# Kernel tuning notes

Measured on AMD Instinct MI355X. Metric: run time of the kernel, lower is better.

## Reference

```python
import jax, jax.numpy as jnp
import numpy as np

N_DRUG = 572
D = 512
K = 64          # neighbor_sample_size
T = 30000       # tail entities
R = 200         # relations
MAX_DEG = 32    # padded invariant_adj neighbor count
EPS = 1e-5


def setup_inputs() -> dict:
    key = jax.random.key(0)
    ks = jax.random.split(key, 10)
    return {
        "drug_embed_W": jax.random.normal(ks[0], (N_DRUG, D), jnp.float32),
        "rela_embed_W": jax.random.normal(ks[1], (R, D), jnp.float32),
        "ent_embed_W": jax.random.normal(ks[2], (T, D), jnp.float32),
        "Wa": jax.random.normal(ks[3], (D, D), jnp.float32) / np.float32(np.sqrt(D)),
        "lin_W": jax.random.normal(ks[4], (2 * D, D), jnp.float32) / np.float32(np.sqrt(2 * D)),
        "lin_b": jnp.zeros((D,), jnp.float32),
        "gamma": jnp.ones((D,), jnp.float32),
        "beta": jnp.zeros((D,), jnp.float32),
        "drug_name": jnp.arange(N_DRUG, dtype=jnp.int64 if jax.config.jax_enable_x64 else jnp.int32),
        "adj_tail": jax.random.randint(ks[5], (N_DRUG, K), 0, T),
        "adj_relation": jax.random.randint(ks[6], (N_DRUG, K), 0, R),
        "nbr_idx": jax.random.randint(ks[7], (N_DRUG, MAX_DEG), 0, N_DRUG),
        "nbr_deg": jax.random.randint(ks[8], (N_DRUG,), 0, MAX_DEG),
        "epoch": 2,
    }


def _forward(drug_embed_W, rela_embed_W, ent_embed_W, Wa, lin_W, lin_b, gamma, beta,
             drug_name, adj_tail, adj_relation, nbr_idx, nbr_deg, epoch):
    drug_e = drug_embed_W[drug_name]          # [N, D]
    rela = rela_embed_W[adj_relation]         # [N, K, D]
    ent = ent_embed_W[adj_tail]               # [N, K, D]

    # relation-aware attention over sampled neighbors (AttentionLayer)
    q = drug_e @ Wa                           # [N, D]
    scores = jnp.einsum('nd,nkd->nk', q, rela) * (1.0 / np.float32(np.sqrt(D)))
    attn = jax.nn.softmax(scores, axis=1)     # [N, K]
    agg = jnp.einsum('nk,nkd->nd', attn, ent) # [N, D]

    # Linear1: Linear(2D->D) + ReLU + BatchNorm1d (training-mode batch stats)
    h = jnp.concatenate([agg, drug_e], axis=1) @ lin_W + lin_b
    h = jax.nn.relu(h)
    mean = jnp.mean(h, axis=0)
    var = jnp.var(h, axis=0)                  # biased, as torch BN normalization
    drug_f = (h - mean) * jax.lax.rsqrt(var + EPS) * gamma + beta

    if epoch > 1:
        # sequential per-node neighbor-mean smoothing (in-place semantics)
        mask = (jnp.arange(MAX_DEG)[None, :] < nbr_deg[:, None])  # [N, MAX_DEG]

        def step(f, i):
            pos = nbr_idx[i]
            m = mask[i][:, None].astype(f.dtype)
            s = jnp.sum(f[pos] * m, axis=0)
            deg = nbr_deg[i]
            avg = s / jnp.maximum(deg, 1).astype(f.dtype)
            new = jnp.where(deg > 0, (avg + f[i]) * 0.5, f[i])
            return f.at[i].set(new), None

        drug_f, _ = jax.lax.scan(step, drug_f, jnp.arange(N_DRUG))
    return drug_f


def reference(drug_embed_W, rela_embed_W, ent_embed_W, Wa, lin_W, lin_b, gamma, beta,
              drug_name, adj_tail, adj_relation, nbr_idx, nbr_deg, epoch):
    return _forward(drug_embed_W, rela_embed_W, ent_embed_W, Wa, lin_W, lin_b, gamma, beta,
                    drug_name, adj_tail, adj_relation, nbr_idx, nbr_deg, epoch)
```

## Files before the change

### kernel.cpp

```cpp
#include <hip/hip_runtime.h>

#define N_DRUG 572
#define DIM 512
#define MAXDEG 32
#define FSB 12

__global__ __launch_bounds__(256) void prep_kernel(
    const float* __restrict__ Wa, const float* __restrict__ relaW,
    const float* __restrict__ linW, const int* __restrict__ nbr_idx,
    const int* __restrict__ nbr_deg, float* __restrict__ linP,
    float* __restrict__ relaP, int* __restrict__ sched_g)
{
    const int b = blockIdx.x;
    const int t = threadIdx.x;
    if (b < 512) {
        const int g = b * 256 + t;
        const int c = g & 511, k4 = g >> 9;
        const float4 v = make_float4(linW[(size_t)(k4 * 4 + 0) * 512 + c],
                                     linW[(size_t)(k4 * 4 + 1) * 512 + c],
                                     linW[(size_t)(k4 * 4 + 2) * 512 + c],
                                     linW[(size_t)(k4 * 4 + 3) * 512 + c]);
        *(float4*)&linP[((size_t)(c >> 6) * 256 + k4) * 256 + (c & 63) * 4] = v;
        return;
    }
    if (b == 928) {
        __shared__ int mxs2[N_DRUG];
        for (int i = t; i < N_DRUG; i += 256) {
            const int d = nbr_deg[i];
            const int4* np = (const int4*)&nbr_idx[i * MAXDEG];
            int mx = -1;
            #pragma unroll
            for (int u = 0; u < 8; ++u) {
                const int4 qq = np[u];
                const int bb = u * 4;
                mx = max(mx, (bb + 0 < d && qq.x < i) ? qq.x : -1);
                mx = max(mx, (bb + 1 < d && qq.y < i) ? qq.y : -1);
                mx = max(mx, (bb + 2 < d && qq.z < i) ? qq.z : -1);
                mx = max(mx, (bb + 3 < d && qq.w < i) ? qq.w : -1);
            }
            mxs2[i] = mx;
        }
        __syncthreads();
        if (t < 64) {
            int gs = 0, nr = 0;
            if (t == 0) sched_g[0] = 0;
            while (gs < N_DRUG) {
                const int jj = gs + 1 + t;
                const bool flag = (t >= 15) || (jj >= N_DRUG) ||
                                  (mxs2[min(jj, N_DRUG - 1)] >= gs);
                const int ge = gs + 1 + (int)__builtin_ctzll(__ballot(flag) & 0xFFFFULL);
                ++nr;
                if (t == 0) sched_g[nr] = ge;
                gs = ge;
            }
            if (t == 0) {
                sched_g[nr + 1] = N_DRUG;
                sched_g[nr + 2] = N_DRUG;
                sched_g[nr + 3] = N_DRUG;
            }
        }
        return;
    }
    const int bb = b - 512;
    const int rb = bb >> 5, kb = bb & 31;
    const int wv = t >> 6, l = t & 63;
    const int r0 = rb * 16 + wv * 4;
    const int k0 = kb * 16;

    float a[4][8];
    #pragma unroll
    for (int rr = 0; rr < 4; ++rr) {
        const float4* ap = (const float4*)(relaW + (size_t)min(r0 + rr, 199) * 512 + l * 8);
        const float4 x = ap[0], y = ap[1];
        a[rr][0] = x.x; a[rr][1] = x.y; a[rr][2] = x.z; a[rr][3] = x.w;
        a[rr][4] = y.x; a[rr][5] = y.y; a[rr][6] = y.z; a[rr][7] = y.w;
    }
    float acc[64];
    #pragma unroll
    for (int i = 0; i < 64; ++i) acc[i] = 0.f;
    #pragma unroll
    for (int kk = 0; kk < 16; ++kk) {
        const float4* bp = (const float4*)(Wa + (size_t)(k0 + kk) * 512 + l * 8);
        const float4 x = bp[0], y = bp[1];
        const float bv[8] = {x.x, x.y, x.z, x.w, y.x, y.y, y.z, y.w};
        #pragma unroll
        for (int rr = 0; rr < 4; ++rr) {
            float s = acc[rr * 16 + kk];
            #pragma unroll
            for (int j = 0; j < 8; ++j) s = fmaf(a[rr][j], bv[j], s);
            acc[rr * 16 + kk] = s;
        }
    }
    #pragma unroll
    for (int off = 1; off <= 32; off <<= 1) {
        #pragma unroll
        for (int i = 0; i < 64; ++i) acc[i] += __shfl_xor(acc[i], off, 64);
    }
    float outv = acc[0];
    #pragma unroll
    for (int i = 1; i < 64; ++i) outv = (l == i) ? acc[i] : outv;
    const int rr = l >> 4, kk = l & 15;
    if (r0 + rr < 200) relaP[(size_t)(r0 + rr) * 512 + k0 + kk] = outv;
}

__global__ __launch_bounds__(256) void attn_kernel(
    const float* __restrict__ drugW, const float* __restrict__ relaP,
    const float* __restrict__ entW, const int* __restrict__ dn,
    const int* __restrict__ adj_tail, const int* __restrict__ adj_rel,
    float* __restrict__ cat)
{
    __shared__ float at[64];
    __shared__ int tails[64];
    __shared__ int rels[64];
    const int d = blockIdx.x;
    const int t = threadIdx.x;
    const int w = t >> 6, lane = t & 63;

    if (t < 64) {
        tails[t] = adj_tail[d * 64 + t];
        rels[t]  = adj_rel[d * 64 + t];
    }
    const int rd = dn[d];
    float qv[8];
    {
        const float4* qp = (const float4*)(drugW + (size_t)rd * 512 + lane * 8);
        const float4 x = qp[0], y = qp[1];
        qv[0] = x.x; qv[1] = x.y; qv[2] = x.z; qv[3] = x.w;
        qv[4] = y.x; qv[5] = y.y; qv[6] = y.z; qv[7] = y.w;
    }
    __syncthreads();

    #pragma unroll 4
    for (int kk = 0; kk < 16; ++kk) {
        const int k = w * 16 + kk;
        const float4* p = (const float4*)(relaP + (size_t)rels[k] * 512 + lane * 8);
        const float4 x = p[0], y = p[1];
        float s = 0.f;
        s = fmaf(qv[0], x.x, s); s = fmaf(qv[1], x.y, s);
        s = fmaf(qv[2], x.z, s); s = fmaf(qv[3], x.w, s);
        s = fmaf(qv[4], y.x, s); s = fmaf(qv[5], y.y, s);
        s = fmaf(qv[6], y.z, s); s = fmaf(qv[7], y.w, s);
        #pragma unroll
        for (int off = 32; off >= 1; off >>= 1) s += __shfl_xor(s, off, 64);
        if (lane == 0) at[k] = s * 0.0441941738241592f;
    }
    __syncthreads();

    if (w == 0) {
        const float s = at[lane];
        float m = s;
        #pragma unroll
        for (int off = 32; off >= 1; off >>= 1) m = fmaxf(m, __shfl_xor(m, off, 64));
        const float e = __expf(s - m);
        float sum = e;
        #pragma unroll
        for (int off = 32; off >= 1; off >>= 1) sum += __shfl_xor(sum, off, 64);
        at[lane] = e / sum;
    }
    __syncthreads();

    {
        const int c2 = t * 2;
        float a0 = 0.f, a1 = 0.f;
        #pragma unroll 8
        for (int k = 0; k < 64; ++k) {
            const float ak = at[k];
            const float2 e = *(const float2*)(entW + (size_t)tails[k] * 512 + c2);
            a0 = fmaf(ak, e.x, a0);
            a1 = fmaf(ak, e.y, a1);
        }
        float* o = cat + (size_t)d * 1024;
        *(float2*)&o[c2] = make_float2(a0, a1);
        const float2 de = *(const float2*)(drugW + (size_t)rd * 512 + c2);
        *(float2*)&o[512 + c2] = de;
    }
}

__global__ __launch_bounds__(512) void gemm_h(
    const float* __restrict__ A, const float* __restrict__ linP,
    const float* __restrict__ bias, float* __restrict__ out)
{
    __shared__ float red[8][8][128];
    const int t = threadIdx.x;
    const int wv = t >> 6, lane = t & 63;
    const int r0 = blockIdx.x * 8;
    const int half = lane >> 5;
    const int cw = (lane * 2) & 63;

    const float* wp = linP + ((size_t)(blockIdx.y * 2 + half) * 256 + wv * 32) * 256
                    + cw * 4;
    const float* ap[8];
    #pragma unroll
    for (int r = 0; r < 8; ++r)
        ap[r] = A + (size_t)min(r0 + r, N_DRUG - 1) * 1024 + wv * 128;

    float acc0[8] = {0.f, 0.f, 0.f, 0.f, 0.f, 0.f, 0.f, 0.f};
    float acc1[8] = {0.f, 0.f, 0.f, 0.f, 0.f, 0.f, 0.f, 0.f};

    float4 wa = *(const float4*)(wp);
    float4 wb = *(const float4*)(wp + 4);
    float4 aa[8];
    #pragma unroll
    for (int r = 0; r < 8; ++r) aa[r] = *(const float4*)(ap[r]);

    for (int k4 = 0; k4 < 32; ++k4) {
        const int kn = (k4 + 1) & 31;
        const float4 wan = *(const float4*)(wp + (size_t)kn * 256);
        const float4 wbn = *(const float4*)(wp + (size_t)kn * 256 + 4);
        float4 an[8];
        #pragma unroll
        for (int r = 0; r < 8; ++r) an[r] = *(const float4*)(ap[r] + kn * 4);

        #pragma unroll
        for (int r = 0; r < 8; ++r) {
            const float4 a = aa[r];
            acc0[r] = fmaf(a.x, wa.x, acc0[r]);
            acc0[r] = fmaf(a.y, wa.y, acc0[r]);
            acc0[r] = fmaf(a.z, wa.z, acc0[r]);
            acc0[r] = fmaf(a.w, wa.w, acc0[r]);
            acc1[r] = fmaf(a.x, wb.x, acc1[r]);
            acc1[r] = fmaf(a.y, wb.y, acc1[r]);
            acc1[r] = fmaf(a.z, wb.z, acc1[r]);
            acc1[r] = fmaf(a.w, wb.w, acc1[r]);
        }
        wa = wan; wb = wbn;
        #pragma unroll
        for (int r = 0; r < 8; ++r) aa[r] = an[r];
    }

    #pragma unroll
    for (int r = 0; r < 8; ++r)
        *(float2*)&red[wv][r][lane * 2] = make_float2(acc0[r], acc1[r]);
    __syncthreads();

    #pragma unroll
    for (int u = 0; u < 2; ++u) {
        const int o = u * 512 + t;
        const int r = o >> 7, cc = o & 127;
        if (r0 + r < N_DRUG) {
            float v = red[0][r][cc];
            #pragma unroll
            for (int w = 1; w < 8; ++w) v += red[w][r][cc];
            v += bias[blockIdx.y * 128 + cc];
            out[(size_t)(r0 + r) * 512 + blockIdx.y * 128 + cc] = fmaxf(v, 0.f);
        }
    }
}

__global__ __launch_bounds__(64) void scan_kernel(
    float* hout, const float* __restrict__ gamma, const float* __restrict__ beta,
    const int* __restrict__ nbr_idx, const int* __restrict__ nbr_deg,
    const int* __restrict__ epoch, const int* __restrict__ sched_g)
{
    __shared__ alignas(16) unsigned char fsb[(N_DRUG + 1) * FSB];
    __shared__ alignas(16) unsigned short offsA[N_DRUG * MAXDEG];
    __shared__ alignas(16) unsigned short offsB[N_DRUG * MAXDEG];
    __shared__ float2 ivw[N_DRUG];
    __shared__ int sched[N_DRUG + 8];

    const int lane = threadIdx.x;
    const int col  = lane & 1;
    const int rg   = lane >> 1;
    const int c0   = blockIdx.x * 2;
    const int cl4  = col * 4;

    for (int i = lane; i < N_DRUG + 8; i += 64) sched[i] = sched_g[i];

    for (int i = lane; i < N_DRUG; i += 64) {
        const int d = nbr_deg[i];
        ivw[i] = (d > 0) ? make_float2(0.5f / (float)d, 0.5f) : make_float2(0.f, 1.f);
        const int4* np = (const int4*)&nbr_idx[i * MAXDEG];
        uint2* opA = (uint2*)&offsA[i * MAXDEG];
        uint2* opB = (uint2*)&offsB[i * MAXDEG];
        #pragma unroll
        for (int u = 0; u < 8; ++u) {
            const int4 qq = np[u];
            const int b = u * 4;
            const int rx = (b + 0 < d) ? qq.x : N_DRUG;
            const int ry = (b + 1 < d) ? qq.y : N_DRUG;
            const int rz = (b + 2 < d) ? qq.z : N_DRUG;
            const int rw = (b + 3 < d) ? qq.w : N_DRUG;
            const unsigned w0 = (unsigned)(rx * FSB) | ((unsigned)(ry * FSB) << 16);
            const unsigned w1 = (unsigned)(rz * FSB) | ((unsigned)(rw * FSB) << 16);
            opA[u] = make_uint2(w0, w1);
            opB[u] = make_uint2(w0 + 0x00040004u, w1 + 0x00040004u);
        }
    }

    float sl = 0.f, ql = 0.f;
    for (int r = rg; r < N_DRUG; r += 32) {
        const float v = hout[(size_t)r * DIM + c0 + col];
        *(float*)(fsb + r * FSB + cl4) = v;
        sl += v;
        ql = fmaf(v, v, ql);
    }
    if (lane < 3) *(float*)(fsb + N_DRUG * FSB + lane * 4) = 0.f;
    #pragma unroll
    for (int off = 2; off <= 32; off <<= 1) {
        sl += __shfl_xor(sl, off, 64);
        ql += __shfl_xor(ql, off, 64);
    }
    const float mean = sl * (1.f / N_DRUG);
    const float var  = ql * (1.f / N_DRUG) - mean * mean;
    const float rstd = rsqrtf(var + 1e-5f);
    const float scl  = gamma[c0 + col] * rstd;
    const float shf  = beta[c0 + col] - mean * scl;

    for (int r = rg; r < N_DRUG; r += 32) {
        float* p = (float*)(fsb + r * FSB + cl4);
        *p = fmaf(*p, scl, shf);
    }

    if (epoch[0] > 1) {
        const int j  = lane >> 2;
        const int hh = (lane >> 1) & 1;
        const unsigned short* obase = col ? offsB : offsA;

        int gs  = 0;
        int ge  = sched[1];
        int ge2 = sched[2];
        int rp  = 3;
        uint4 ca, cb;
        {
            const uint4* p = (const uint4*)&obase[j * MAXDEG + hh * 16];
            ca = p[0]; cb = p[1];
        }
        float  cur = *(const float*)(fsb + j * FSB + cl4);
        float2 iw  = ivw[j];

        while (gs < N_DRUG) {
            const bool pred = (gs + j) < ge;
            float s0 = 0.f, s1 = 0.f;
            if (pred) {
#define G2(W) { s0 += *(const float*)(fsb + (W & 0xffffu)); \
                s1 += *(const float*)(fsb + (W >> 16)); }
                G2(ca.x) G2(ca.y) G2(ca.z) G2(ca.w)
                G2(cb.x) G2(cb.y) G2(cb.z) G2(cb.w)
#undef G2
            }
            uint4 na, nb;
            {
                const uint4* p = (const uint4*)&obase[min(ge + j, N_DRUG - 1) * MAXDEG + hh * 16];
                na = p[0]; nb = p[1];
            }
            const float  ncur = *(const float*)(fsb + min(ge + j, N_DRUG) * FSB + cl4);
            const float2 niw  = ivw[min(ge + j, N_DRUG - 1)];
            const int    nge  = sched[rp];

            float nv = 0.f;
            if (pred) {
                float sh = s0 + s1;
                sh += __int_as_float(__builtin_amdgcn_mov_dpp(
                          __float_as_int(sh), 0x4E, 0xF, 0xF, false));
                nv = fmaf(sh, iw.x, cur * iw.y);
            }
            asm volatile("" ::: "memory");
            if (pred && hh == 0) *(float*)(fsb + (gs + j) * FSB + cl4) = nv;
            asm volatile("" ::: "memory");
            gs = ge; ge = ge2; ge2 = nge; ++rp;
            ca = na; cb = nb; cur = ncur; iw = niw;
        }
    }

    for (int r = rg; r < N_DRUG; r += 32)
        hout[(size_t)r * DIM + c0 + col] = *(const float*)(fsb + r * FSB + cl4);
}

extern "C" void kernel_launch(void* const* d_in, const int* in_sizes, int n_in,
                              void* d_out, int out_size, void* d_ws, size_t ws_size,
                              hipStream_t stream)
{
    const float* drugW = (const float*)d_in[0];
    const float* relaW = (const float*)d_in[1];
    const float* entW  = (const float*)d_in[2];
    const float* Wa    = (const float*)d_in[3];
    const float* linW  = (const float*)d_in[4];
    const float* linb  = (const float*)d_in[5];
    const float* gamma = (const float*)d_in[6];
    const float* beta  = (const float*)d_in[7];
    const int* drug_name = (const int*)d_in[8];
    const int* adj_tail  = (const int*)d_in[9];
    const int* adj_rel   = (const int*)d_in[10];
    const int* nbr_idx   = (const int*)d_in[11];
    const int* nbr_deg   = (const int*)d_in[12];
    const int* epoch     = (const int*)d_in[13];

    float* out = (float*)d_out;

    float* linP   = (float*)d_ws;
    float* relaP  = (float*)((char*)d_ws + 2097152);
    float* cat    = (float*)((char*)d_ws + 2506752);
    int*   sched  = (int*)  ((char*)d_ws + 4849664);

    prep_kernel<<<929, 256, 0, stream>>>(Wa, relaW, linW, nbr_idx, nbr_deg,
                                         linP, relaP, sched);
    attn_kernel<<<N_DRUG, 256, 0, stream>>>(drugW, relaP, entW, drug_name,
                                            adj_tail, adj_rel, cat);
    gemm_h<<<dim3(72, 4), 512, 0, stream>>>(cat, linP, linb, out);
    scan_kernel<<<256, 64, 0, stream>>>(out, gamma, beta, nbr_idx, nbr_deg,
                                        epoch, sched);
}
```

Measured before the change: 224.0 us.

## Schedule sequential smoothing by dependency levels and split attention aggregation over k

Replaces the contiguous-run scheduling of the sequential neighbor-smoothing scan with a level-based topological schedule. Each node's level is computed by iterative relaxation over its lower-indexed neighbors, and nodes are grouped by level into rounds of up to 16. The scan kernel keeps original and updated values in two shared buffers so higher-indexed neighbors read pre-update values, which should cut the number of serial rounds. The attention aggregation also splits the 64 neighbors across two thread halves, uses float4 loads and combines the halves through shared memory. In exchange, prep does extra serial work (up to 600 relaxation iterations and a single-thread histogram scan) and the scan kernel uses more shared memory.

```diff
diff --git a/kernel.cpp b/kernel.cpp
--- a/kernel.cpp
+++ b/kernel.cpp
@@ -4,6 +4,9 @@
 #define DIM 512
 #define MAXDEG 32
 #define FSB 12
+#define ORIG_OFF (573 * FSB)
+#define DUMMY_ORIG (ORIG_OFF + 572 * FSB)
+#define SLOTS 588
 
 __global__ __launch_bounds__(256) void prep_kernel(
     const float* __restrict__ Wa, const float* __restrict__ relaW,
@@ -24,40 +27,63 @@
         return;
     }
     if (b == 928) {
-        __shared__ int mxs2[N_DRUG];
+        __shared__ unsigned short lowN[N_DRUG * MAXDEG];
+        __shared__ unsigned char  lowC[N_DRUG];
+        __shared__ short lvl[N_DRUG];
+        __shared__ int hist[N_DRUG];
+        __shared__ int off0[N_DRUG];
+        __shared__ int cntL[N_DRUG];
+        __shared__ int chg;
+
         for (int i = t; i < N_DRUG; i += 256) {
             const int d = nbr_deg[i];
             const int4* np = (const int4*)&nbr_idx[i * MAXDEG];
-            int mx = -1;
+            int c = 0;
+            unsigned short* lp = &lowN[i * MAXDEG];
             #pragma unroll
             for (int u = 0; u < 8; ++u) {
                 const int4 qq = np[u];
                 const int bb = u * 4;
-                mx = max(mx, (bb + 0 < d && qq.x < i) ? qq.x : -1);
-                mx = max(mx, (bb + 1 < d && qq.y < i) ? qq.y : -1);
-                mx = max(mx, (bb + 2 < d && qq.z < i) ? qq.z : -1);
-                mx = max(mx, (bb + 3 < d && qq.w < i) ? qq.w : -1);
-            }
-            mxs2[i] = mx;
+                if (bb + 0 < d && qq.x < i) lp[c++] = (unsigned short)qq.x;
+                if (bb + 1 < d && qq.y < i) lp[c++] = (unsigned short)qq.y;
+                if (bb + 2 < d && qq.z < i) lp[c++] = (unsigned short)qq.z;
+                if (bb + 3 < d && qq.w < i) lp[c++] = (unsigned short)qq.w;
+            }
+            lowC[i] = (unsigned char)c;
+            lvl[i] = 0;
+            hist[i] = 0; cntL[i] = 0;
         }
         __syncthreads();
-        if (t < 64) {
-            int gs = 0, nr = 0;
-            if (t == 0) sched_g[0] = 0;
-            while (gs < N_DRUG) {
-                const int jj = gs + 1 + t;
-                const bool flag = (t >= 15) || (jj >= N_DRUG) ||
-                                  (mxs2[min(jj, N_DRUG - 1)] >= gs);
-                const int ge = gs + 1 + (int)__builtin_ctzll(__ballot(flag) & 0xFFFFULL);
-                ++nr;
-                if (t == 0) sched_g[nr] = ge;
-                gs = ge;
-            }
-            if (t == 0) {
-                sched_g[nr + 1] = N_DRUG;
-                sched_g[nr + 2] = N_DRUG;
-                sched_g[nr + 3] = N_DRUG;
-            }
+        for (int it = 0; it < 600; ++it) {
+            if (t == 0) chg = 0;
+            __syncthreads();
+            for (int i = t; i < N_DRUG; i += 256) {
+                const int c = lowC[i];
+                int m = -1;
+                for (int u = 0; u < c; ++u) m = max(m, (int)lvl[lowN[i * MAXDEG + u]]);
+                if (m + 1 > (int)lvl[i]) { lvl[i] = (short)(m + 1); chg = 1; }
+            }
+            __syncthreads();
+            if (!chg) break;
+        }
+        for (int i = t; i < N_DRUG; i += 256) atomicAdd(&hist[lvl[i]], 1);
+        __syncthreads();
+        if (t == 0) {
+            int acc = 0, nr = 0;
+            for (int L = 0; L < N_DRUG; ++L) {
+                off0[L] = acc;
+                int w = hist[L];
+                acc += w;
+                while (w > 0) { const int c = min(w, 16); sched_g[573 + nr] = c; ++nr; w -= c; }
+            }
+            sched_g[0] = nr;
+            sched_g[573 + nr] = 0;
+            sched_g[573 + nr + 1] = 0;
+        }
+        __syncthreads();
+        for (int i = t; i < N_DRUG; i += 256) {
+            const int p = off0[lvl[i]] + atomicAdd(&cntL[lvl[i]], 1);
+            sched_g[1 + p] = i;
         }
         return;
     }
@@ -112,6 +138,7 @@
     __shared__ float at[64];
     __shared__ int tails[64];
     __shared__ int rels[64];
+    __shared__ float part[512];
     const int d = blockIdx.x;
     const int t = threadIdx.x;
     const int w = t >> 6, lane = t & 63;
@@ -160,19 +187,26 @@
     __syncthreads();
 
     {
-        const int c2 = t * 2;
-        float a0 = 0.f, a1 = 0.f;
+        const int kh = t >> 7;
+        const int c4 = (t & 127) * 4;
+        float a0 = 0.f, a1 = 0.f, a2 = 0.f, a3 = 0.f;
         #pragma unroll 8
-        for (int k = 0; k < 64; ++k) {
+        for (int kk = 0; kk < 32; ++kk) {
+            const int k = kh * 32 + kk;
             const float ak = at[k];
-            const float2 e = *(const float2*)(entW + (size_t)tails[k] * 512 + c2);
-            a0 = fmaf(ak, e.x, a0);
-            a1 = fmaf(ak, e.y, a1);
-        }
-        float* o = cat + (size_t)d * 1024;
-        *(float2*)&o[c2] = make_float2(a0, a1);
-        const float2 de = *(const float2*)(drugW + (size_t)rd * 512 + c2);
-        *(float2*)&o[512 + c2] = de;
+            const float4 e = *(const float4*)(entW + (size_t)tails[k] * 512 + c4);
+            a0 = fmaf(ak, e.x, a0); a1 = fmaf(ak, e.y, a1);
+            a2 = fmaf(ak, e.z, a2); a3 = fmaf(ak, e.w, a3);
+        }
+        if (kh == 1) *(float4*)&part[c4] = make_float4(a0, a1, a2, a3);
+        __syncthreads();
+        if (kh == 0) {
+            const float4 p = *(const float4*)&part[c4];
+            float* o = cat + (size_t)d * 1024;
+            *(float4*)&o[c4] = make_float4(a0 + p.x, a1 + p.y, a2 + p.z, a3 + p.w);
+            const float4 de = *(const float4*)(drugW + (size_t)rd * 512 + c4);
+            *(float4*)&o[512 + c4] = de;
+        }
     }
 }
 
@@ -252,11 +286,12 @@
     const int* __restrict__ nbr_idx, const int* __restrict__ nbr_deg,
     const int* __restrict__ epoch, const int* __restrict__ sched_g)
 {
-    __shared__ alignas(16) unsigned char fsb[(N_DRUG + 1) * FSB];
-    __shared__ alignas(16) unsigned short offsA[N_DRUG * MAXDEG];
-    __shared__ alignas(16) unsigned short offsB[N_DRUG * MAXDEG];
-    __shared__ float2 ivw[N_DRUG];
-    __shared__ int sched[N_DRUG + 8];
+    __shared__ alignas(16) unsigned char fsb[2 * ORIG_OFF + 16];
+    __shared__ alignas(16) unsigned short offsPA[SLOTS * MAXDEG];
+    __shared__ alignas(16) unsigned short offsPB[SLOTS * MAXDEG];
+    __shared__ float2 ivwP[SLOTS];
+    __shared__ unsigned short selfP[SLOTS];
+    __shared__ int rcnt[576];
 
     const int lane = threadIdx.x;
     const int col  = lane & 1;
@@ -264,37 +299,60 @@
     const int c0   = blockIdx.x * 2;
     const int cl4  = col * 4;
 
-    for (int i = lane; i < N_DRUG + 8; i += 64) sched[i] = sched_g[i];
-
-    for (int i = lane; i < N_DRUG; i += 64) {
-        const int d = nbr_deg[i];
-        ivw[i] = (d > 0) ? make_float2(0.5f / (float)d, 0.5f) : make_float2(0.f, 1.f);
-        const int4* np = (const int4*)&nbr_idx[i * MAXDEG];
-        uint2* opA = (uint2*)&offsA[i * MAXDEG];
-        uint2* opB = (uint2*)&offsB[i * MAXDEG];
-        #pragma unroll
-        for (int u = 0; u < 8; ++u) {
-            const int4 qq = np[u];
-            const int b = u * 4;
-            const int rx = (b + 0 < d) ? qq.x : N_DRUG;
-            const int ry = (b + 1 < d) ? qq.y : N_DRUG;
-            const int rz = (b + 2 < d) ? qq.z : N_DRUG;
-            const int rw = (b + 3 < d) ? qq.w : N_DRUG;
-            const unsigned w0 = (unsigned)(rx * FSB) | ((unsigned)(ry * FSB) << 16);
-            const unsigned w1 = (unsigned)(rz * FSB) | ((unsigned)(rw * FSB) << 16);
-            opA[u] = make_uint2(w0, w1);
-            opB[u] = make_uint2(w0 + 0x00040004u, w1 + 0x00040004u);
+    const int nrounds = sched_g[0];
+    for (int i = lane; i < 576; i += 64) rcnt[i] = (i < nrounds) ? sched_g[573 + i] : 0;
+
+    for (int s = lane; s < SLOTS; s += 64) {
+        const int node = (s < N_DRUG) ? sched_g[1 + s] : N_DRUG;
+        uint2* opA = (uint2*)&offsPA[s * MAXDEG];
+        uint2* opB = (uint2*)&offsPB[s * MAXDEG];
+        if (node < N_DRUG) {
+            const int d = nbr_deg[node];
+            ivwP[s] = (d > 0) ? make_float2(0.5f / (float)d, 0.5f)
+                              : make_float2(0.f, 1.f);
+            selfP[s] = (unsigned short)(node * FSB);
+            const int4* np = (const int4*)&nbr_idx[node * MAXDEG];
+            #pragma unroll
+            for (int u = 0; u < 8; ++u) {
+                const int4 qq = np[u];
+                const int b = u * 4;
+                unsigned o[4];
+                const int nn[4] = {qq.x, qq.y, qq.z, qq.w};
+                #pragma unroll
+                for (int e = 0; e < 4; ++e) {
+                    const int nbr = nn[e];
+                    o[e] = (b + e < d)
+                         ? (unsigned)((nbr >= node ? ORIG_OFF : 0) + nbr * FSB)
+                         : (unsigned)DUMMY_ORIG;
+                }
+                const unsigned w0 = o[0] | (o[1] << 16);
+                const unsigned w1 = o[2] | (o[3] << 16);
+                opA[u] = make_uint2(w0, w1);
+                opB[u] = make_uint2(w0 + 0x00040004u, w1 + 0x00040004u);
+            }
+        } else {
+            ivwP[s] = make_float2(0.f, 1.f);
+            selfP[s] = (unsigned short)(N_DRUG * FSB);
+            #pragma unroll
+            for (int u = 0; u < 8; ++u) {
+                const unsigned wd = (unsigned)DUMMY_ORIG | ((unsigned)DUMMY_ORIG << 16);
+                opA[u] = make_uint2(wd, wd);
+                opB[u] = make_uint2(wd + 0x00040004u, wd + 0x00040004u);
+            }
         }
     }
 
     float sl = 0.f, ql = 0.f;
     for (int r = rg; r < N_DRUG; r += 32) {
         const float v = hout[(size_t)r * DIM + c0 + col];
-        *(float*)(fsb + r * FSB + cl4) = v;
+        *(float*)(fsb + ORIG_OFF + r * FSB + cl4) = v;
         sl += v;
         ql = fmaf(v, v, ql);
     }
-    if (lane < 3) *(float*)(fsb + N_DRUG * FSB + lane * 4) = 0.f;
+    if (lane < 3) {
+        *(float*)(fsb + N_DRUG * FSB + lane * 4) = 0.f;
+        *(float*)(fsb + ORIG_OFF + N_DRUG * FSB + lane * 4) = 0.f;
+    }
     #pragma unroll
     for (int off = 2; off <= 32; off <<= 1) {
         sl += __shfl_xor(sl, off, 64);
@@ -307,29 +365,31 @@
     const float shf  = beta[c0 + col] - mean * scl;
 
     for (int r = rg; r < N_DRUG; r += 32) {
-        float* p = (float*)(fsb + r * FSB + cl4);
+        float* p = (float*)(fsb + ORIG_OFF + r * FSB + cl4);
         *p = fmaf(*p, scl, shf);
     }
 
-    if (epoch[0] > 1) {
+    const bool smooth = (epoch[0] > 1);
+    if (smooth) {
         const int j  = lane >> 2;
         const int hh = (lane >> 1) & 1;
-        const unsigned short* obase = col ? offsB : offsA;
-
-        int gs  = 0;
-        int ge  = sched[1];
-        int ge2 = sched[2];
-        int rp  = 3;
+        const unsigned short* obase = col ? offsPB : offsPA;
+
+        int base = 0;
+        int cnt  = rcnt[0];
+        int nct  = rcnt[1];
+        int rp   = 2;
         uint4 ca, cb;
         {
             const uint4* p = (const uint4*)&obase[j * MAXDEG + hh * 16];
             ca = p[0]; cb = p[1];
         }
-        float  cur = *(const float*)(fsb + j * FSB + cl4);
-        float2 iw  = ivw[j];
-
-        while (gs < N_DRUG) {
-            const bool pred = (gs + j) < ge;
+        unsigned scur = selfP[j];
+        float  cur = *(const float*)(fsb + ORIG_OFF + scur + cl4);
+        float2 iw  = ivwP[j];
+
+        while (base < N_DRUG) {
+            const bool pred = j < cnt;
             float s0 = 0.f, s1 = 0.f;
             if (pred) {
 #define G2(W) { s0 += *(const float*)(fsb + (W & 0xffffu)); \
@@ -338,14 +398,16 @@
                 G2(cb.x) G2(cb.y) G2(cb.z) G2(cb.w)
 #undef G2
             }
+            const int nbase = base + cnt;
             uint4 na, nb;
             {
-                const uint4* p = (const uint4*)&obase[min(ge + j, N_DRUG - 1) * MAXDEG + hh * 16];
+                const uint4* p = (const uint4*)&obase[(nbase + j) * MAXDEG + hh * 16];
                 na = p[0]; nb = p[1];
             }
-            const float  ncur = *(const float*)(fsb + min(ge + j, N_DRUG) * FSB + cl4);
-            const float2 niw  = ivw[min(ge + j, N_DRUG - 1)];
-            const int    nge  = sched[rp];
+            const unsigned nscur = selfP[nbase + j];
+            const float  ncur = *(const float*)(fsb + ORIG_OFF + nscur + cl4);
+            const float2 niw  = ivwP[nbase + j];
+            const int    nnct = rcnt[rp];
 
             float nv = 0.f;
             if (pred) {
@@ -355,15 +417,16 @@
                 nv = fmaf(sh, iw.x, cur * iw.y);
             }
             asm volatile("" ::: "memory");
-            if (pred && hh == 0) *(float*)(fsb + (gs + j) * FSB + cl4) = nv;
+            if (pred && hh == 0) *(float*)(fsb + scur + cl4) = nv;
             asm volatile("" ::: "memory");
-            gs = ge; ge = ge2; ge2 = nge; ++rp;
-            ca = na; cb = nb; cur = ncur; iw = niw;
-        }
-    }
-
+            base = nbase; cnt = nct; nct = nnct; ++rp;
+            ca = na; cb = nb; scur = nscur; cur = ncur; iw = niw;
+        }
+    }
+
+    const int rb = smooth ? 0 : ORIG_OFF;
     for (int r = rg; r < N_DRUG; r += 32)
-        hout[(size_t)r * DIM + c0 + col] = *(const float*)(fsb + r * FSB + cl4);
+        hout[(size_t)r * DIM + c0 + col] = *(const float*)(fsb + rb + r * FSB + cl4);
 }
 
 extern "C" void kernel_launch(void* const* d_in, const int* in_sizes, int n_in,
```

After: 336.1 us. 1.5x slower.
